# Kernel optimization log

Hardware: AMD Instinct MI355X
Metric: run time of the kernel (lower is better)

Reference implementation:

```python
import jax, jax.numpy as jnp
import numpy as np

B, T, C, H = 4, 2048, 1024, 16
D = C // H  # head_size = 64


def setup_inputs() -> dict:
    key = jax.random.key(0)
    k1, k2, k3 = jax.random.split(key, 3)
    s = 1.0 / np.sqrt(C)
    return {
        "x": jax.random.normal(k1, (B, T, C), dtype=jnp.float32),
        "w_qkv": jax.random.normal(k2, (3 * C, C), dtype=jnp.float32) * s,
        "w_out": jax.random.normal(k3, (C, C), dtype=jnp.float32) * s,
        "b_out": jnp.zeros((C,), dtype=jnp.float32),
    }


def reference(x, w_qkv, w_out, b_out):
    Bx, Tx, Cx = x.shape
    qkv = x @ w_qkv.T                                # [B,T,3C]
    q, k, v = jnp.split(qkv, 3, axis=2)
    # [B,T,C] -> [B,H,T,D]
    q = q.reshape(Bx, Tx, H, D).transpose(0, 2, 1, 3)
    k = k.reshape(Bx, Tx, H, D).transpose(0, 2, 1, 3)
    v = v.reshape(Bx, Tx, H, D).transpose(0, 2, 1, 3)
    scores = jnp.einsum('bhqd,bhkd->bhqk', q, k) / jnp.sqrt(jnp.float32(D))
    causal = jnp.tril(jnp.ones((Tx, Tx), dtype=bool))
    scores = jnp.where(causal[None, None], scores, -jnp.inf)
    attn = jax.nn.softmax(scores, axis=-1)
    out = jnp.einsum('bhqk,bhkd->bhqd', attn, v)     # [B,H,T,D]
    out = out.transpose(0, 2, 1, 3).reshape(Bx, Tx, Cx)
    return out @ w_out.T + b_out
```

## Files before the change

kernel.cpp:

```cpp
#include <hip/hip_runtime.h>

constexpr int Bn = 4, Tn = 2048, Cn = 1024, Hn = 16, Dn = 64;

typedef __attribute__((ext_vector_type(8))) short short8;
typedef __attribute__((ext_vector_type(4))) float floatx4;
typedef __attribute__((ext_vector_type(2))) unsigned uint2v;

#define DEVFN __device__ __forceinline__

constexpr float SCL = 0.18033688011112042f;

DEVFN unsigned f2bf_u(float f) {
  unsigned u = __builtin_bit_cast(unsigned, f);
  u += 0x7fffu + ((u >> 16) & 1u);
  return u >> 16;
}
DEVFN short f2bf(float f) { return (short)f2bf_u(f); }

DEVFN floatx4 mfma16(short8 a, short8 b, floatx4 c) {
  return __builtin_amdgcn_mfma_f32_16x16x32_bf16(a, b, c, 0, 0, 0);
}

DEVFN void gld_lds16(const void* g, void* l) {
  __builtin_amdgcn_global_load_lds(
      (const __attribute__((address_space(1))) unsigned*)g,
      (__attribute__((address_space(3))) unsigned*)l, 16, 0, 0);
}

constexpr int G_X = 8192 * 1024 / 8;
constexpr int G_WQ = 3072 * 1024 / 8;
constexpr int G_WO = 1024 * 1024 / 8;
__global__ __launch_bounds__(256) void cast3_kernel(
    const float* __restrict__ x, const float* __restrict__ wq,
    const float* __restrict__ wo, short* __restrict__ dst) {
  const int i = blockIdx.x * 256 + threadIdx.x;
  const float* src;
  int rel;
  if (i < G_X) {
    src = x; rel = i;
  } else if (i < G_X + G_WQ) {
    src = wq; rel = i - G_X;
  } else {
    src = wo; rel = i - (G_X + G_WQ);
  }
  const floatx4* p = (const floatx4*)src + (size_t)rel * 2;
  floatx4 a = p[0], b = p[1];
  short8 r;
  r[0] = f2bf(a[0]); r[1] = f2bf(a[1]); r[2] = f2bf(a[2]); r[3] = f2bf(a[3]);
  r[4] = f2bf(b[0]); r[5] = f2bf(b[1]); r[6] = f2bf(b[2]); r[7] = f2bf(b[3]);
  ((short8*)dst)[i] = r;
}

template <int MODE>
__global__ __launch_bounds__(256, 2) void gemm_bt(
    const short* __restrict__ A, const short* __restrict__ Bw, int M, int N, int K,
    short* __restrict__ qkb, short* __restrict__ vtb,
    const float* __restrict__ bias, float* __restrict__ fout) {
  __shared__ short As[128 * 64];
  __shared__ short Bs[128 * 64];
  const int tid = threadIdx.x;
  const int lane = tid & 63, wave = tid >> 6;
  const int l15 = lane & 15, quad = lane >> 4;
  const int wr = wave >> 1, wc = wave & 1;
  const int m0 = blockIdx.x * 128, n0 = blockIdx.y * 128;

  const int r0 = tid >> 3, cs = tid & 7;
  const short* Ag = A + (size_t)(m0 + r0) * K + (cs ^ (r0 & 7)) * 8;
  const short* Bg = Bw + (size_t)(n0 + r0) * K + (cs ^ (r0 & 7)) * 8;

  floatx4 acc[4][4] = {};

  for (int k0 = 0; k0 < K; k0 += 64) {
#pragma unroll
    for (int it = 0; it < 4; ++it) {
      gld_lds16(Ag + k0 + (size_t)(it * 32) * K, As + it * 2048 + tid * 8);
      gld_lds16(Bg + k0 + (size_t)(it * 32) * K, Bs + it * 2048 + tid * 8);
    }
    __syncthreads();
#pragma unroll
    for (int ks = 0; ks < 2; ++ks) {
      short8 af[4], bf[4];
#pragma unroll
      for (int i = 0; i < 4; ++i) {
        const int row = wr * 64 + i * 16 + l15;
        af[i] = *(const short8*)(As + row * 64 +
                                 ((ks * 4 + quad) ^ (l15 & 7)) * 8);
      }
#pragma unroll
      for (int i = 0; i < 4; ++i) {
        const int row = wc * 64 + i * 16 + l15;
        bf[i] = *(const short8*)(Bs + row * 64 +
                                 ((ks * 4 + quad) ^ (l15 & 7)) * 8);
      }
#pragma unroll
      for (int mi = 0; mi < 4; ++mi)
#pragma unroll
        for (int ni = 0; ni < 4; ++ni)
          acc[mi][ni] = mfma16(af[mi], bf[ni], acc[mi][ni]);
    }
    __syncthreads();
  }

#pragma unroll
  for (int mi = 0; mi < 4; ++mi) {
    const int row0 = m0 + wr * 64 + mi * 16 + quad * 4;
#pragma unroll
    for (int ni = 0; ni < 4; ++ni) {
      const int col = n0 + wc * 64 + ni * 16 + l15;
      if constexpr (MODE == 0) {
        if (col < 2 * Cn) {
#pragma unroll
          for (int r = 0; r < 4; ++r) {
            float v = acc[mi][ni][r];
            if (col < Cn) v *= SCL;
            qkb[(size_t)(row0 + r) * (2 * Cn) + col] = f2bf(v);
          }
        } else {
          const int hc = col - 2 * Cn;
          const int hh = hc >> 6, d = hc & 63;
          const int bb = row0 >> 11, t = row0 & (Tn - 1);
          uint2v pk;
          pk[0] = f2bf_u(acc[mi][ni][0]) | (f2bf_u(acc[mi][ni][1]) << 16);
          pk[1] = f2bf_u(acc[mi][ni][2]) | (f2bf_u(acc[mi][ni][3]) << 16);
          *(uint2v*)(vtb + ((size_t)((bb * Hn + hh) * Dn + d)) * Tn + t) = pk;
        }
      } else {
#pragma unroll
        for (int r = 0; r < 4; ++r)
          fout[(size_t)(row0 + r) * N + col] = acc[mi][ni][r] + bias[col];
      }
    }
  }
}

__global__ __launch_bounds__(256, 3) void attn_kernel(
    const short* __restrict__ qk, const short* __restrict__ vt,
    short* __restrict__ att) {
  __shared__ short Ks[2][64 * 64];
  __shared__ short Vs[2][64 * 64];
  __shared__ short Ps[4][16 * 64];

  const int bh = blockIdx.x;
  const int qt = 15 - blockIdx.y;
  const int b = bh >> 4, h = bh & 15;
  const int tid = threadIdx.x;
  const int lane = tid & 63, wave = tid >> 6;
  const int l15 = lane & 15, quad = lane >> 4;
  const int q0w = qt * 128 + wave * 32;

  const short* qbase = qk + (size_t)(b * Tn) * 2048 + h * 64;
  const short* kbase = qbase + 1024;
  const short* vbase = vt + (size_t)(bh * 64) * Tn;
  short* pw = Ps[wave];

  short8 qf[2][2];
#pragma unroll
  for (int f = 0; f < 2; ++f)
#pragma unroll
    for (int ks = 0; ks < 2; ++ks)
      qf[f][ks] = *(const short8*)(qbase + (size_t)(q0w + f * 16 + l15) * 2048 +
                                   ks * 32 + quad * 8);

  floatx4 o[2][4] = {};
  float lpart[2] = {0.f, 0.f};

  const int wave_nt = ((q0w + 31) >> 6) + 1;
  const int block_nt = 2 * qt + 2;

  const int jr = tid >> 3;
  const int cl = tid & 7;

#define STAGE(JT, BUF)                                                       \
  {                                                                          \
    const int j0s = (JT) * 64;                                               \
    _Pragma("unroll") for (int it = 0; it < 2; ++it) {                       \
      const int row = jr + it * 32;                                          \
      const int cg = cl ^ (row & 7);                                         \
      gld_lds16(kbase + (size_t)(j0s + row) * 2048 + cg * 8,                 \
                &Ks[BUF][it * 2048 + tid * 8]);                              \
      gld_lds16(vbase + (size_t)row * Tn + j0s + cg * 8,                     \
                &Vs[BUF][it * 2048 + tid * 8]);                              \
    }                                                                        \
  }

  STAGE(0, 0)
  __syncthreads();

  for (int jt = 0; jt < block_nt; ++jt) {
    const int buf = jt & 1;
    if (jt + 1 < block_nt) STAGE(jt + 1, buf ^ 1)

    if (jt < wave_nt) {
      const int j0 = jt * 64;

      floatx4 st[2][4];
#pragma unroll
      for (int f = 0; f < 2; ++f)
#pragma unroll
        for (int nj = 0; nj < 4; ++nj) st[f][nj] = floatx4{0.f, 0.f, 0.f, 0.f};
#pragma unroll
      for (int half = 0; half < 2; ++half) {
        short8 kfa[2][2];
#pragma unroll
        for (int j2 = 0; j2 < 2; ++j2)
#pragma unroll
          for (int ks = 0; ks < 2; ++ks) {
            const int cld = (ks * 4 + quad) ^ (l15 & 7);
            kfa[j2][ks] = *(const short8*)(
                &Ks[buf][((half * 2 + j2) * 16 + l15) * 64 + cld * 8]);
          }
#pragma unroll
        for (int f = 0; f < 2; ++f)
#pragma unroll
          for (int j2 = 0; j2 < 2; ++j2)
#pragma unroll
            for (int ks = 0; ks < 2; ++ks)
              st[f][half * 2 + j2] =
                  mfma16(kfa[j2][ks], qf[f][ks], st[f][half * 2 + j2]);
      }

      short8 vf[4][2];
#pragma unroll
      for (int nd = 0; nd < 4; ++nd)
#pragma unroll
        for (int ks = 0; ks < 2; ++ks) {
          const int cld = (ks * 4 + quad) ^ (l15 & 7);
          vf[nd][ks] =
              *(const short8*)(&Vs[buf][(nd * 16 + l15) * 64 + cld * 8]);
        }

#pragma unroll
      for (int f = 0; f < 2; ++f) {
        const bool need_mask = (j0 + 63 > q0w + f * 16);
        const int ig = q0w + f * 16 + l15;
#pragma unroll
        for (int nj = 0; nj < 4; ++nj) {
          float p[4];
#pragma unroll
          for (int r = 0; r < 4; ++r) {
            float e = __builtin_amdgcn_exp2f(st[f][nj][r]);
            if (need_mask) {
              const int jg = j0 + nj * 16 + quad * 4 + r;
              e = (jg > ig) ? 0.f : e;
            }
            lpart[f] += e;
            p[r] = e;
          }
          const int c = nj * 2 + (quad >> 1);
          const int cld = c ^ (l15 & 7);
          uint2v pk;
          pk[0] = f2bf_u(p[0]) | (f2bf_u(p[1]) << 16);
          pk[1] = f2bf_u(p[2]) | (f2bf_u(p[3]) << 16);
          *(uint2v*)(&pw[l15 * 64 + cld * 8 + (quad & 1) * 4]) = pk;
        }
        __asm__ volatile("s_waitcnt lgkmcnt(0)" ::: "memory");

        short8 pf[2];
#pragma unroll
        for (int ks = 0; ks < 2; ++ks) {
          const int cld = (ks * 4 + quad) ^ (l15 & 7);
          pf[ks] = *(const short8*)(&pw[l15 * 64 + cld * 8]);
        }
#pragma unroll
        for (int nd = 0; nd < 4; ++nd)
#pragma unroll
          for (int ks = 0; ks < 2; ++ks)
            o[f][nd] = mfma16(vf[nd][ks], pf[ks], o[f][nd]);
        __asm__ volatile("" ::: "memory");
      }
    }
    __syncthreads();
  }

  float inv[2];
#pragma unroll
  for (int f = 0; f < 2; ++f) {
    float s2 = lpart[f];
    s2 += __shfl_xor(s2, 16);
    s2 += __shfl_xor(s2, 32);
    inv[f] = 1.0f / s2;
  }

#pragma unroll
  for (int f = 0; f < 2; ++f) {
#pragma unroll
    for (int nd = 0; nd < 4; ++nd) {
      const int c = nd * 2 + (quad >> 1);
      const int cld = c ^ (l15 & 7);
      uint2v pk;
      pk[0] =
          f2bf_u(o[f][nd][0] * inv[f]) | (f2bf_u(o[f][nd][1] * inv[f]) << 16);
      pk[1] =
          f2bf_u(o[f][nd][2] * inv[f]) | (f2bf_u(o[f][nd][3] * inv[f]) << 16);
      *(uint2v*)(&pw[l15 * 64 + cld * 8 + (quad & 1) * 4]) = pk;
    }
    __asm__ volatile("s_waitcnt lgkmcnt(0)" ::: "memory");
#pragma unroll
    for (int ps = 0; ps < 2; ++ps) {
      const int r16 = ps * 8 + (lane >> 3);
      const int cn = lane & 7;
      const int cldr = cn ^ (r16 & 7);
      const short8 val = *(const short8*)(&pw[r16 * 64 + cldr * 8]);
      *(short8*)(att + (size_t)(b * Tn + q0w + f * 16 + r16) * Cn + h * 64 +
                 cn * 8) = val;
    }
    __asm__ volatile("" ::: "memory");
  }
#undef STAGE
}

extern "C" void kernel_launch(void* const* d_in, const int* in_sizes, int n_in,
                              void* d_out, int out_size, void* d_ws,
                              size_t ws_size, hipStream_t stream) {
  const float* x = (const float*)d_in[0];
  const float* w_qkv = (const float*)d_in[1];
  const float* w_out = (const float*)d_in[2];
  const float* b_out = (const float*)d_in[3];
  float* out = (float*)d_out;

  short* xb = (short*)d_ws;
  short* wqb = xb + (size_t)8192 * 1024;
  short* wob = wqb + (size_t)3072 * 1024;
  short* qkb = wob + (size_t)1024 * 1024;
  short* vtb = qkb + (size_t)8192 * 2048;
  short* att = xb;

  cast3_kernel<<<dim3((G_X + G_WQ + G_WO) / 256), 256, 0, stream>>>(
      x, w_qkv, w_out, xb);

  gemm_bt<0><<<dim3(64, 24), 256, 0, stream>>>(xb, wqb, 8192, 3072, 1024, qkb,
                                               vtb, nullptr, nullptr);
  attn_kernel<<<dim3(64, 16), 256, 0, stream>>>(qkb, vtb, att);
  gemm_bt<1><<<dim3(64, 8), 256, 0, stream>>>(att, wob, 8192, 1024, 1024,
                                              nullptr, nullptr, b_out, out);
}
```

Baseline: 229.2 us.

## Enlarge attention query tile to 256 rows and use cheaper bf16 packing

Each attention block now processes 256 query rows (64 per wave) instead of 128, so every K/V tile staged in LDS feeds four query fragments per wave and total K/V loads are halved. K fragments are loaded once per tile and score MFMAs are computed per fragment, with launch bounds relaxed to 2 blocks per CU for more registers. Block ordering interleaves long and short causal tiles, and bf16 packing uses an add-and-permute instead of round-to-nearest-even. Risks include higher register pressure, fewer blocks for occupancy, and slightly different rounding.

```diff
diff --git a/kernel.cpp b/kernel.cpp
--- a/kernel.cpp
+++ b/kernel.cpp
@@ -16,6 +16,12 @@
   return u >> 16;
 }
 DEVFN short f2bf(float f) { return (short)f2bf_u(f); }
+
+DEVFN unsigned pack_bf16(float a, float b) {
+  unsigned ua = __builtin_bit_cast(unsigned, a) + 0x8000u;
+  unsigned ub = __builtin_bit_cast(unsigned, b) + 0x8000u;
+  return __builtin_amdgcn_perm(ub, ua, 0x07060302u);
+}
 
 DEVFN floatx4 mfma16(short8 a, short8 b, floatx4 c) {
   return __builtin_amdgcn_mfma_f32_16x16x32_bf16(a, b, c, 0, 0, 0);
@@ -133,7 +139,7 @@
   }
 }
 
-__global__ __launch_bounds__(256, 3) void attn_kernel(
+__global__ __launch_bounds__(256, 2) void attn_kernel(
     const short* __restrict__ qk, const short* __restrict__ vt,
     short* __restrict__ att) {
   __shared__ short Ks[2][64 * 64];
@@ -141,31 +147,32 @@
   __shared__ short Ps[4][16 * 64];
 
   const int bh = blockIdx.x;
-  const int qt = 15 - blockIdx.y;
+  const int y = blockIdx.y;
+  const int qt = (y < 4) ? (7 - y) : (y - 4);
   const int b = bh >> 4, h = bh & 15;
   const int tid = threadIdx.x;
   const int lane = tid & 63, wave = tid >> 6;
   const int l15 = lane & 15, quad = lane >> 4;
-  const int q0w = qt * 128 + wave * 32;
+  const int q0w = qt * 256 + wave * 64;
 
   const short* qbase = qk + (size_t)(b * Tn) * 2048 + h * 64;
   const short* kbase = qbase + 1024;
   const short* vbase = vt + (size_t)(bh * 64) * Tn;
   short* pw = Ps[wave];
 
-  short8 qf[2][2];
-#pragma unroll
-  for (int f = 0; f < 2; ++f)
+  short8 qf[4][2];
+#pragma unroll
+  for (int f = 0; f < 4; ++f)
 #pragma unroll
     for (int ks = 0; ks < 2; ++ks)
       qf[f][ks] = *(const short8*)(qbase + (size_t)(q0w + f * 16 + l15) * 2048 +
                                    ks * 32 + quad * 8);
 
-  floatx4 o[2][4] = {};
-  float lpart[2] = {0.f, 0.f};
-
-  const int wave_nt = ((q0w + 31) >> 6) + 1;
-  const int block_nt = 2 * qt + 2;
+  floatx4 o[4][4] = {};
+  float lpart[4] = {};
+
+  const int wave_nt = 4 * qt + wave + 1;
+  const int block_nt = 4 * qt + 4;
 
   const int jr = tid >> 3;
   const int cl = tid & 7;
@@ -193,44 +200,29 @@
     if (jt < wave_nt) {
       const int j0 = jt * 64;
 
-      floatx4 st[2][4];
-#pragma unroll
-      for (int f = 0; f < 2; ++f)
-#pragma unroll
-        for (int nj = 0; nj < 4; ++nj) st[f][nj] = floatx4{0.f, 0.f, 0.f, 0.f};
-#pragma unroll
-      for (int half = 0; half < 2; ++half) {
-        short8 kfa[2][2];
-#pragma unroll
-        for (int j2 = 0; j2 < 2; ++j2)
-#pragma unroll
-          for (int ks = 0; ks < 2; ++ks) {
-            const int cld = (ks * 4 + quad) ^ (l15 & 7);
-            kfa[j2][ks] = *(const short8*)(
-                &Ks[buf][((half * 2 + j2) * 16 + l15) * 64 + cld * 8]);
-          }
-#pragma unroll
-        for (int f = 0; f < 2; ++f)
-#pragma unroll
-          for (int j2 = 0; j2 < 2; ++j2)
-#pragma unroll
-            for (int ks = 0; ks < 2; ++ks)
-              st[f][half * 2 + j2] =
-                  mfma16(kfa[j2][ks], qf[f][ks], st[f][half * 2 + j2]);
-      }
-
-      short8 vf[4][2];
-#pragma unroll
-      for (int nd = 0; nd < 4; ++nd)
+      short8 kf[4][2], vf[4][2];
+#pragma unroll
+      for (int nj = 0; nj < 4; ++nj)
 #pragma unroll
         for (int ks = 0; ks < 2; ++ks) {
           const int cld = (ks * 4 + quad) ^ (l15 & 7);
-          vf[nd][ks] =
-              *(const short8*)(&Vs[buf][(nd * 16 + l15) * 64 + cld * 8]);
-        }
-
-#pragma unroll
-      for (int f = 0; f < 2; ++f) {
+          kf[nj][ks] =
+              *(const short8*)(&Ks[buf][(nj * 16 + l15) * 64 + cld * 8]);
+          vf[nj][ks] =
+              *(const short8*)(&Vs[buf][(nj * 16 + l15) * 64 + cld * 8]);
+        }
+
+#pragma unroll
+      for (int f = 0; f < 4; ++f) {
+        floatx4 st[4];
+#pragma unroll
+        for (int nj = 0; nj < 4; ++nj) {
+          st[nj] = floatx4{0.f, 0.f, 0.f, 0.f};
+#pragma unroll
+          for (int ks = 0; ks < 2; ++ks)
+            st[nj] = mfma16(kf[nj][ks], qf[f][ks], st[nj]);
+        }
+
         const bool need_mask = (j0 + 63 > q0w + f * 16);
         const int ig = q0w + f * 16 + l15;
 #pragma unroll
@@ -238,7 +230,7 @@
           float p[4];
 #pragma unroll
           for (int r = 0; r < 4; ++r) {
-            float e = __builtin_amdgcn_exp2f(st[f][nj][r]);
+            float e = __builtin_amdgcn_exp2f(st[nj][r]);
             if (need_mask) {
               const int jg = j0 + nj * 16 + quad * 4 + r;
               e = (jg > ig) ? 0.f : e;
@@ -249,8 +241,8 @@
           const int c = nj * 2 + (quad >> 1);
           const int cld = c ^ (l15 & 7);
           uint2v pk;
-          pk[0] = f2bf_u(p[0]) | (f2bf_u(p[1]) << 16);
-          pk[1] = f2bf_u(p[2]) | (f2bf_u(p[3]) << 16);
+          pk[0] = pack_bf16(p[0], p[1]);
+          pk[1] = pack_bf16(p[2], p[3]);
           *(uint2v*)(&pw[l15 * 64 + cld * 8 + (quad & 1) * 4]) = pk;
         }
         __asm__ volatile("s_waitcnt lgkmcnt(0)" ::: "memory");
@@ -272,9 +264,9 @@
     __syncthreads();
   }
 
-  float inv[2];
-#pragma unroll
-  for (int f = 0; f < 2; ++f) {
+  float inv[4];
+#pragma unroll
+  for (int f = 0; f < 4; ++f) {
     float s2 = lpart[f];
     s2 += __shfl_xor(s2, 16);
     s2 += __shfl_xor(s2, 32);
@@ -282,16 +274,14 @@
   }
 
 #pragma unroll
-  for (int f = 0; f < 2; ++f) {
+  for (int f = 0; f < 4; ++f) {
 #pragma unroll
     for (int nd = 0; nd < 4; ++nd) {
       const int c = nd * 2 + (quad >> 1);
       const int cld = c ^ (l15 & 7);
       uint2v pk;
-      pk[0] =
-          f2bf_u(o[f][nd][0] * inv[f]) | (f2bf_u(o[f][nd][1] * inv[f]) << 16);
-      pk[1] =
-          f2bf_u(o[f][nd][2] * inv[f]) | (f2bf_u(o[f][nd][3] * inv[f]) << 16);
+      pk[0] = pack_bf16(o[f][nd][0] * inv[f], o[f][nd][1] * inv[f]);
+      pk[1] = pack_bf16(o[f][nd][2] * inv[f], o[f][nd][3] * inv[f]);
       *(uint2v*)(&pw[l15 * 64 + cld * 8 + (quad & 1) * 4]) = pk;
     }
     __asm__ volatile("s_waitcnt lgkmcnt(0)" ::: "memory");
@@ -330,7 +320,7 @@
 
   gemm_bt<0><<<dim3(64, 24), 256, 0, stream>>>(xb, wqb, 8192, 3072, 1024, qkb,
                                                vtb, nullptr, nullptr);
-  attn_kernel<<<dim3(64, 16), 256, 0, stream>>>(qkb, vtb, att);
+  attn_kernel<<<dim3(64, 8), 256, 0, stream>>>(qkb, vtb, att);
   gemm_bt<1><<<dim3(64, 8), 256, 0, stream>>>(att, wob, 8192, 1024, 1024,
                                               nullptr, nullptr, b_out, out);
 }
```

After: 266.0 us. 16.1% more time.
